# Kernel optimization log

Hardware: AMD Instinct MI355X
Metric: run time of the kernel (lower is better)

## Reference

```python
import jax, jax.numpy as jnp
import numpy as np

D_K = 64
SCALE = 1.0 / (D_K ** 0.5)
NEG = -1.0e9

def setup_inputs() -> dict:
    key = jax.random.key(0)
    kq, kk, kv, km = jax.random.split(key, 4)
    B, H, S, D = 4, 16, 2048, D_K
    query = jax.random.normal(kq, (B, H, S, D), dtype=jnp.float32)
    k_ = jax.random.normal(kk, (B, H, S, D), dtype=jnp.float32)
    v_ = jax.random.normal(kv, (B, H, S, D), dtype=jnp.float32)
    mask = jax.random.randint(km, (B, 1, S, S), 0, 2, dtype=jnp.int32)
    return {"query": query, "key": k_, "value": v_, "mask": mask}

def reference(query, key, value, mask):
    # scores: [B, H, S, S]
    scores = jnp.einsum('bhqd,bhkd->bhqk', query, key) * SCALE
    scores = jnp.where(mask == 0, NEG, scores)
    attn = jax.nn.softmax(scores, axis=-1)
    return jnp.einsum('bhqk,bhkd->bhqd', attn, value)
```

## Files before the change

### kernel.cpp

```cpp
#include <hip/hip_runtime.h>

typedef _Float16 f16x8 __attribute__((ext_vector_type(8)));
typedef _Float16 f16x4 __attribute__((ext_vector_type(4)));
typedef _Float16 f16x2 __attribute__((ext_vector_type(2)));
typedef float    f32x4 __attribute__((ext_vector_type(4)));
typedef unsigned u32x4 __attribute__((ext_vector_type(4)));
typedef unsigned long long u64;

constexpr int Bc = 4, Hc = 16, Sc = 2048, Dc = 64;
constexpr int KVBLK = 64;
constexpr int NKV = Sc / KVBLK;
constexpr int QB  = 256;
constexpr int NQT = Sc / QB;
constexpr int NQ  = 32;

__device__ __forceinline__ float fast_exp2(float x) {
#if __has_builtin(__builtin_amdgcn_exp2f)
  return __builtin_amdgcn_exp2f(x);
#else
  return exp2f(x);
#endif
}

__device__ __forceinline__ void gload16(const void* g, void* l) {
  __builtin_amdgcn_global_load_lds(
      (const __attribute__((address_space(1))) void*)g,
      (__attribute__((address_space(3))) void*)l, 16, 0, 0);
}

__device__ __forceinline__ f32x4 mfma16(f16x8 a, f16x8 b, f32x4 c) {
  return __builtin_amdgcn_mfma_f32_16x16x32_f16(a, b, c, 0, 0, 0);
}

__device__ __forceinline__ unsigned pkrtz(float x, float y) {
  return __builtin_bit_cast(unsigned, __builtin_amdgcn_cvt_pkrtz(x, y));
}

__device__ __forceinline__ float dot2acc(unsigned pk, float acc) {
#if __has_builtin(__builtin_amdgcn_fdot2)
  const f16x2 one2 = {(_Float16)1.f, (_Float16)1.f};
  return __builtin_amdgcn_fdot2(__builtin_bit_cast(f16x2, pk), one2, acc, false);
#else
  const f16x2 v = __builtin_bit_cast(f16x2, pk);
  return acc + (float)v[0] + (float)v[1];
#endif
}

__global__ __launch_bounds__(256)
void cvt_k_sw(const float* __restrict__ K, _Float16* __restrict__ Ko) {
  const int tile = blockIdx.x;
  const int t = threadIdx.x;
  const float* src = K + (size_t)tile * 4096;
  _Float16* dst = Ko + (size_t)tile * 4096;
  #pragma unroll
  for (int cc = 0; cc < 2; ++cc) {
    const int c = t + cc * 256;
    const int r = c >> 3, s = c & 7;
    const int ss = s ^ (r & 7);
    const float* p = src + r * 64 + ss * 8;
    const float4 a = *(const float4*)p;
    const float4 b2 = *(const float4*)(p + 4);
    f16x8 h = {(_Float16)a.x, (_Float16)a.y, (_Float16)a.z, (_Float16)a.w,
               (_Float16)b2.x, (_Float16)b2.y, (_Float16)b2.z, (_Float16)b2.w};
    *(f16x8*)(dst + (size_t)c * 8) = h;
  }
}

__global__ __launch_bounds__(256)
void cvt_v_sw(const float* __restrict__ V, _Float16* __restrict__ Vo) {
  __shared__ float tile[64][65];
  const int tb = blockIdx.x;
  const int t = threadIdx.x;
  const float* src = V + (size_t)tb * 4096;
  {
    const int r = t >> 2, c0 = (t & 3) * 16;
    #pragma unroll
    for (int j = 0; j < 16; j += 4)
      *(float4*)&tile[r][c0 + j] = *(const float4*)(src + r * 64 + c0 + j);
  }
  __syncthreads();
  _Float16* dst = Vo + (size_t)tb * 4096;
  #pragma unroll
  for (int cc = 0; cc < 2; ++cc) {
    const int c = t + cc * 256;
    const int d = c >> 3, ss = c & 7;
    const int m = ss ^ (d & 7);
    const int ks = m >> 2, lg = m & 3;
    f16x8 h;
    #pragma unroll
    for (int e = 0; e < 8; ++e) {
      const int key = 32 * ks + 16 * (e >> 2) + 4 * lg + (e & 3);
      h[e] = (_Float16)tile[key][d];
    }
    *(f16x8*)(dst + (size_t)c * 8) = h;
  }
}

__global__ __launch_bounds__(256)
void pack_mask(const int* __restrict__ M, u64* __restrict__ MB) {
  const int gid  = blockIdx.x * 256 + threadIdx.x;
  const int wv   = gid >> 6, lane = gid & 63;
  const int kv   = wv & (NKV - 1);
  const int row  = (wv >> 5) & (Sc - 1);
  const int b    = wv >> 16;
  const int m    = M[((size_t)b * Sc + row) * Sc + (size_t)kv * 64 + lane];
  const u64 bits = __ballot(m != 0);
  if (lane == 0)
    MB[(((size_t)b * NQ + (row >> 6)) * NKV + kv) * 64 + (row & 63)] = bits;
}

__global__ __launch_bounds__(512, 4)
void attn_fwd11(const float* __restrict__ Q, const _Float16* __restrict__ Ksw,
                const _Float16* __restrict__ Vsw, const u64* __restrict__ MB,
                float* __restrict__ O)
{
  const int bid = (blockIdx.x & 7) * 64 + (blockIdx.x >> 3);
  const int qt  = bid & (NQT - 1);
  const int bh  = bid >> 3;
  const int b   = bh >> 4;
  const int q0  = qt * QB;

  const int tid = threadIdx.x;
  const int w   = tid >> 6;
  const int l   = tid & 63;
  const int lg  = l >> 4;
  const int lc  = l & 15;

  __shared__ _Float16 SB[16384];
  const char* sb = (const char*)SB;

  const int a0 = lc * 128 + (((0 + lg) ^ (lc & 7)) << 4);
  const int a1 = lc * 128 + (((4 + lg) ^ (lc & 7)) << 4);

  f16x8 qf[2][2];
  {
    const float qs = 0.125f * 1.4426950408889634f;
    #pragma unroll
    for (int qa = 0; qa < 2; ++qa) {
      const float* qr = Q + ((size_t)bh * Sc + q0 + w * 32 + qa * 16 + lc) * Dc + 8 * lg;
      #pragma unroll
      for (int ks = 0; ks < 2; ++ks) {
        f16x8 t;
        #pragma unroll
        for (int e = 0; e < 8; ++e) t[e] = (_Float16)(qr[ks * 32 + e] * qs);
        qf[qa][ks] = t;
      }
    }
  }

  f32x4 o_acc[2][4];
  #pragma unroll
  for (int qa = 0; qa < 2; ++qa)
    #pragma unroll
    for (int nt = 0; nt < 4; ++nt) o_acc[qa][nt] = (f32x4){0.f, 0.f, 0.f, 0.f};
  float l_acc0 = 0.f, l_acc1 = 0.f;
  const float NEGL = -1.4426950e9f;

  const char* KswT = (const char*)(Ksw + (size_t)bh * Sc * Dc);
  const char* VswT = (const char*)(Vsw + (size_t)bh * Sc * Dc);
  const int row0 = q0 + w * 32 + lc;
  const int row1 = row0 + 16;
  const u64* Mb0 = MB + ((size_t)(b * NQ + (row0 >> 6)) * NKV) * 64 + (row0 & 63);
  const u64* Mb1 = MB + ((size_t)(b * NQ + (row1 >> 6)) * NKV) * 64 + (row1 & 63);

  auto stage = [&](int kvt, int buf) {
    const char* g = (w < 4) ? KswT + (size_t)kvt * 8192 + w * 2048
                            : VswT + (size_t)kvt * 8192 + (w - 4) * 2048;
    char* lb = (char*)SB + buf * 16384 + ((w < 4) ? w * 2048 : 8192 + (w - 4) * 2048);
    gload16(g + l * 16, lb);
    gload16(g + 1024 + l * 16, lb + 1024);
  };

  auto body = [&](int buf, u64 m0, u64 m1) {
    const int base = buf * 16384;
    f32x4 p[2][4];
    __builtin_amdgcn_s_setprio(1);
    #pragma unroll
    for (int nt = 0; nt < 4; ++nt) {
      const f16x8 k0 = *(const f16x8*)(sb + base + nt * 2048 + a0);
      const f16x8 k1 = *(const f16x8*)(sb + base + nt * 2048 + a1);
      #pragma unroll
      for (int qa = 0; qa < 2; ++qa) {
        f32x4 acc = (f32x4){0.f, 0.f, 0.f, 0.f};
        acc = mfma16(k0, qf[qa][0], acc);
        acc = mfma16(k1, qf[qa][1], acc);
        p[qa][nt] = acc;
      }
    }
    __builtin_amdgcn_s_setprio(0);
    #pragma unroll
    for (int qa = 0; qa < 2; ++qa) {
      const u64 mbits = qa ? m1 : m0;
      #pragma unroll
      for (int nt = 0; nt < 4; ++nt) {
        const unsigned b4 = ((unsigned)(mbits >> (nt * 16 + 4 * lg))) & 0xFu;
        #pragma unroll
        for (int r = 0; r < 4; ++r)
          p[qa][nt][r] = fast_exp2(((b4 >> r) & 1u) ? p[qa][nt][r] : NEGL);
      }
    }
    f16x8 pa0[2], pa1[2];
    #pragma unroll
    for (int qa = 0; qa < 2; ++qa) {
      u32x4 u0, u1;
      #pragma unroll
      for (int i = 0; i < 4; ++i) {
        u0[i] = pkrtz(p[qa][i >> 1][(i & 1) * 2], p[qa][i >> 1][(i & 1) * 2 + 1]);
        u1[i] = pkrtz(p[qa][2 + (i >> 1)][(i & 1) * 2], p[qa][2 + (i >> 1)][(i & 1) * 2 + 1]);
      }
      float la = qa ? l_acc1 : l_acc0;
      #pragma unroll
      for (int i = 0; i < 4; ++i) { la = dot2acc(u0[i], la); la = dot2acc(u1[i], la); }
      if (qa) l_acc1 = la; else l_acc0 = la;
      pa0[qa] = __builtin_bit_cast(f16x8, u0);
      pa1[qa] = __builtin_bit_cast(f16x8, u1);
    }
    __builtin_amdgcn_s_setprio(1);
    #pragma unroll
    for (int nt = 0; nt < 4; ++nt) {
      const f16x8 v0 = *(const f16x8*)(sb + base + 8192 + nt * 2048 + a0);
      const f16x8 v1 = *(const f16x8*)(sb + base + 8192 + nt * 2048 + a1);
      o_acc[0][nt] = mfma16(pa0[0], v0, o_acc[0][nt]);
      o_acc[0][nt] = mfma16(pa1[0], v1, o_acc[0][nt]);
      o_acc[1][nt] = mfma16(pa0[1], v0, o_acc[1][nt]);
      o_acc[1][nt] = mfma16(pa1[1], v1, o_acc[1][nt]);
    }
    __builtin_amdgcn_s_setprio(0);
  };

  u64 mA0 = Mb0[0], mA1 = Mb1[0];
  stage(0, 0);
  asm volatile("s_waitcnt vmcnt(0)" ::: "memory");
  __builtin_amdgcn_sched_barrier(0);
  __builtin_amdgcn_s_barrier();

  u64 mB0, mB1;
  for (int t = 0; t < NKV; t += 2) {
    stage(t + 1, 1);
    mB0 = Mb0[(size_t)(t + 1) * 64];
    mB1 = Mb1[(size_t)(t + 1) * 64];
    asm volatile("s_waitcnt vmcnt(4)" ::: "memory");
    __builtin_amdgcn_sched_barrier(0);
    __builtin_amdgcn_s_barrier();
    body(0, mA0, mA1);
    __builtin_amdgcn_s_barrier();

    if (t + 2 < NKV) {
      stage(t + 2, 0);
      mA0 = Mb0[(size_t)(t + 2) * 64];
      mA1 = Mb1[(size_t)(t + 2) * 64];
      asm volatile("s_waitcnt vmcnt(4)" ::: "memory");
    } else {
      asm volatile("s_waitcnt vmcnt(0)" ::: "memory");
    }
    __builtin_amdgcn_sched_barrier(0);
    __builtin_amdgcn_s_barrier();
    body(1, mB0, mB1);
    __builtin_amdgcn_s_barrier();
  }

  l_acc0 += __shfl_xor(l_acc0, 16, 64);
  l_acc0 += __shfl_xor(l_acc0, 32, 64);
  l_acc1 += __shfl_xor(l_acc1, 16, 64);
  l_acc1 += __shfl_xor(l_acc1, 32, 64);
  #pragma unroll
  for (int qa = 0; qa < 2; ++qa) {
    #pragma unroll
    for (int r = 0; r < 4; ++r) {
      const float li = 1.0f / __shfl(qa ? l_acc1 : l_acc0, 4 * lg + r, 64);
      float* orow = O + ((size_t)bh * Sc + q0 + w * 32 + qa * 16 + 4 * lg + r) * Dc + lc;
      #pragma unroll
      for (int nt = 0; nt < 4; ++nt)
        orow[nt * 16] = o_acc[qa][nt][r] * li;
    }
  }
}

constexpr int LDSW = KVBLK + 8;

__global__ __launch_bounds__(256)
void attn_fwd_v1(const float* __restrict__ Q, const float* __restrict__ K,
                 const float* __restrict__ V, const int* __restrict__ M,
                 float* __restrict__ O)
{
  const int bid   = blockIdx.x;
  const int qtile = bid & 31;
  const int bh    = bid >> 5;
  const int b     = bh >> 4;

  const float* Qp = Q + ((size_t)bh * Sc + (size_t)qtile * 64) * Dc;
  const float* Kp = K + (size_t)bh * Sc * Dc;
  const float* Vp = V + (size_t)bh * Sc * Dc;
  const int*   Mp = M + (size_t)b * Sc * Sc + (size_t)qtile * 64 * Sc;
  float*       Op = O + ((size_t)bh * Sc + (size_t)qtile * 64) * Dc;

  __shared__ _Float16 Klds [KVBLK][LDSW];
  __shared__ _Float16 Vtlds[Dc]   [LDSW];
  __shared__ _Float16 Pl   [64]   [LDSW];

  const int tid = threadIdx.x;
  const int w   = tid >> 6;
  const int l   = tid & 63;
  const int lg  = l >> 4;
  const int lc  = l & 15;

  f16x8 qf[2];
  {
    const float qs = 0.125f * 1.4426950408889634f;
    const float* qrow = Qp + (size_t)(w * 16 + lc) * Dc + 8 * lg;
    #pragma unroll
    for (int ks = 0; ks < 2; ++ks) {
      f16x8 t;
      #pragma unroll
      for (int e = 0; e < 8; ++e) t[e] = (_Float16)(qrow[ks * 32 + e] * qs);
      qf[ks] = t;
    }
  }

  f32x4 o_acc[4];
  #pragma unroll
  for (int nt = 0; nt < 4; ++nt) o_acc[nt] = (f32x4){0.f, 0.f, 0.f, 0.f};
  float m_r[4], l_r[4];
  #pragma unroll
  for (int r = 0; r < 4; ++r) { m_r[r] = -3.0e38f; l_r[r] = 0.f; }
  const float NEGL = -1.4426950e9f;

  for (int kv = 0; kv < NKV; ++kv) {
    const float* Kt = Kp + (size_t)kv * KVBLK * Dc;
    const float* Vt = Vp + (size_t)kv * KVBLK * Dc;
    __syncthreads();
    {
      const int r = tid >> 2, c0 = (tid & 3) * 16;
      const float* src = Kt + (size_t)r * Dc + c0;
      f16x8 h0, h1;
      #pragma unroll
      for (int e = 0; e < 8; ++e) h0[e] = (_Float16)src[e];
      #pragma unroll
      for (int e = 0; e < 8; ++e) h1[e] = (_Float16)src[8 + e];
      *(f16x8*)&Klds[r][c0]     = h0;
      *(f16x8*)&Klds[r][c0 + 8] = h1;
    }
    {
      const int r0 = (tid >> 4) * 4, c0 = (tid & 15) * 4;
      float a_[4][4];
      #pragma unroll
      for (int i = 0; i < 4; ++i) {
        const float4 v4 = *(const float4*)(Vt + (size_t)(r0 + i) * Dc + c0);
        a_[i][0] = v4.x; a_[i][1] = v4.y; a_[i][2] = v4.z; a_[i][3] = v4.w;
      }
      #pragma unroll
      for (int j = 0; j < 4; ++j) {
        f16x4 t = {(_Float16)a_[0][j], (_Float16)a_[1][j],
                   (_Float16)a_[2][j], (_Float16)a_[3][j]};
        *(f16x4*)&Vtlds[c0 + j][r0] = t;
      }
    }
    __syncthreads();

    f32x4 s_acc[4];
    #pragma unroll
    for (int nt = 0; nt < 4; ++nt) {
      f32x4 acc = (f32x4){0.f, 0.f, 0.f, 0.f};
      #pragma unroll
      for (int ks = 0; ks < 2; ++ks) {
        f16x8 kf = *(const f16x8*)&Klds[nt * 16 + lc][ks * 32 + 8 * lg];
        acc = __builtin_amdgcn_mfma_f32_16x16x32_f16(qf[ks], kf, acc, 0, 0, 0);
      }
      s_acc[nt] = acc;
    }

    const int* mbase = Mp + (size_t)kv * KVBLK + lc;
    #pragma unroll
    for (int r = 0; r < 4; ++r) {
      const int qrow = w * 16 + 4 * lg + r;
      const int* mr = mbase + (size_t)qrow * Sc;
      float s0 = (mr[0]  != 0) ? s_acc[0][r] : NEGL;
      float s1 = (mr[16] != 0) ? s_acc[1][r] : NEGL;
      float s2 = (mr[32] != 0) ? s_acc[2][r] : NEGL;
      float s3 = (mr[48] != 0) ? s_acc[3][r] : NEGL;
      float mx = fmaxf(fmaxf(s0, s1), fmaxf(s2, s3));
      #pragma unroll
      for (int off = 1; off < 16; off <<= 1)
        mx = fmaxf(mx, __shfl_xor(mx, off, 64));
      const float mn   = fmaxf(m_r[r], mx);
      const float corr = fast_exp2(m_r[r] - mn);
      m_r[r] = mn;
      float p0 = fast_exp2(s0 - mn);
      float p1 = fast_exp2(s1 - mn);
      float p2 = fast_exp2(s2 - mn);
      float p3 = fast_exp2(s3 - mn);
      float rs = (p0 + p1) + (p2 + p3);
      #pragma unroll
      for (int off = 1; off < 16; off <<= 1)
        rs += __shfl_xor(rs, off, 64);
      l_r[r] = l_r[r] * corr + rs;
      #pragma unroll
      for (int nt = 0; nt < 4; ++nt) o_acc[nt][r] *= corr;
      Pl[qrow][lc]      = (_Float16)p0;
      Pl[qrow][16 + lc] = (_Float16)p1;
      Pl[qrow][32 + lc] = (_Float16)p2;
      Pl[qrow][48 + lc] = (_Float16)p3;
    }

    #pragma unroll
    for (int nt = 0; nt < 4; ++nt) {
      #pragma unroll
      for (int ks = 0; ks < 2; ++ks) {
        f16x8 pf = *(const f16x8*)&Pl[w * 16 + lc][ks * 32 + 8 * lg];
        f16x8 vf = *(const f16x8*)&Vtlds[nt * 16 + lc][ks * 32 + 8 * lg];
        o_acc[nt] = __builtin_amdgcn_mfma_f32_16x16x32_f16(pf, vf, o_acc[nt], 0, 0, 0);
      }
    }
  }

  #pragma unroll
  for (int r = 0; r < 4; ++r) {
    const float inv = 1.0f / l_r[r];
    float* orow = Op + (size_t)(w * 16 + 4 * lg + r) * Dc;
    #pragma unroll
    for (int nt = 0; nt < 4; ++nt)
      orow[nt * 16 + lc] = o_acc[nt][r] * inv;
  }
}

extern "C" void kernel_launch(void* const* d_in, const int* in_sizes, int n_in,
                              void* d_out, int out_size, void* d_ws, size_t ws_size,
                              hipStream_t stream) {
  (void)in_sizes; (void)n_in; (void)out_size;
  const float* Q = (const float*)d_in[0];
  const float* K = (const float*)d_in[1];
  const float* V = (const float*)d_in[2];
  const int*   M = (const int*)d_in[3];
  float*       O = (float*)d_out;

  const size_t nKV      = (size_t)Bc * Hc * Sc * Dc;
  const size_t bytesK16 = nKV * 2;
  const size_t bytesMB  = (size_t)Bc * NQ * NKV * 64 * 8;
  const size_t need     = 2 * bytesK16 + bytesMB;

  if (ws_size >= need) {
    _Float16* K16  = (_Float16*)d_ws;
    _Float16* Vt16 = (_Float16*)((char*)d_ws + bytesK16);
    u64*      MBp  = (u64*)((char*)d_ws + 2 * bytesK16);
    hipLaunchKernelGGL(cvt_k_sw,   dim3(2048),  dim3(256), 0, stream, K, K16);
    hipLaunchKernelGGL(cvt_v_sw,   dim3(2048),  dim3(256), 0, stream, V, Vt16);
    hipLaunchKernelGGL(pack_mask,  dim3(65536), dim3(256), 0, stream, M, MBp);
    hipLaunchKernelGGL(attn_fwd11, dim3(512),   dim3(512), 0, stream, Q, K16, Vt16, MBp, O);
  } else {
    hipLaunchKernelGGL(attn_fwd_v1, dim3(2048), dim3(256), 0, stream, Q, K, V, M, O);
  }
}
```

Baseline: 130.2 us.

## Process 64 query rows per wave with 4-wave blocks to raise K/V reuse

Each block now runs 4 waves instead of 8, and each wave handles 64 query rows (four 16-row groups) instead of 32. Each K/V fragment read from LDS therefore feeds twice as many MFMAs, and every wave stages 4 chunks per tile instead of 2. The aim is to halve LDS read traffic per FLOP and cut barrier and wave overhead. The cost is roughly double the accumulator and score registers per wave and fewer waves to hide latency. The mask loads now use one pointer per wave, covering its 64-row block, instead of one per 16-row group.

```diff
diff --git a/kernel.cpp b/kernel.cpp
--- a/kernel.cpp
+++ b/kernel.cpp
@@ -109,8 +109,8 @@
     MB[(((size_t)b * NQ + (row >> 6)) * NKV + kv) * 64 + (row & 63)] = bits;
 }
 
-__global__ __launch_bounds__(512, 4)
-void attn_fwd11(const float* __restrict__ Q, const _Float16* __restrict__ Ksw,
+__global__ __launch_bounds__(256, 2)
+void attn_fwd13(const float* __restrict__ Q, const _Float16* __restrict__ Ksw,
                 const _Float16* __restrict__ Vsw, const u64* __restrict__ MB,
                 float* __restrict__ O)
 {
@@ -132,12 +132,12 @@
   const int a0 = lc * 128 + (((0 + lg) ^ (lc & 7)) << 4);
   const int a1 = lc * 128 + (((4 + lg) ^ (lc & 7)) << 4);
 
-  f16x8 qf[2][2];
+  f16x8 qf[4][2];
   {
     const float qs = 0.125f * 1.4426950408889634f;
     #pragma unroll
-    for (int qa = 0; qa < 2; ++qa) {
-      const float* qr = Q + ((size_t)bh * Sc + q0 + w * 32 + qa * 16 + lc) * Dc + 8 * lg;
+    for (int qa = 0; qa < 4; ++qa) {
+      const float* qr = Q + ((size_t)bh * Sc + q0 + w * 64 + qa * 16 + lc) * Dc + 8 * lg;
       #pragma unroll
       for (int ks = 0; ks < 2; ++ks) {
         f16x8 t;
@@ -148,39 +148,37 @@
     }
   }
 
-  f32x4 o_acc[2][4];
-  #pragma unroll
-  for (int qa = 0; qa < 2; ++qa)
+  f32x4 o_acc[4][4];
+  #pragma unroll
+  for (int qa = 0; qa < 4; ++qa)
     #pragma unroll
     for (int nt = 0; nt < 4; ++nt) o_acc[qa][nt] = (f32x4){0.f, 0.f, 0.f, 0.f};
-  float l_acc0 = 0.f, l_acc1 = 0.f;
+  float l_acc[4] = {0.f, 0.f, 0.f, 0.f};
   const float NEGL = -1.4426950e9f;
 
   const char* KswT = (const char*)(Ksw + (size_t)bh * Sc * Dc);
   const char* VswT = (const char*)(Vsw + (size_t)bh * Sc * Dc);
-  const int row0 = q0 + w * 32 + lc;
-  const int row1 = row0 + 16;
-  const u64* Mb0 = MB + ((size_t)(b * NQ + (row0 >> 6)) * NKV) * 64 + (row0 & 63);
-  const u64* Mb1 = MB + ((size_t)(b * NQ + (row1 >> 6)) * NKV) * 64 + (row1 & 63);
+  const u64* Mb = MB + ((size_t)(b * NQ + (q0 >> 6) + w) * NKV) * 64 + lc;
 
   auto stage = [&](int kvt, int buf) {
-    const char* g = (w < 4) ? KswT + (size_t)kvt * 8192 + w * 2048
-                            : VswT + (size_t)kvt * 8192 + (w - 4) * 2048;
-    char* lb = (char*)SB + buf * 16384 + ((w < 4) ? w * 2048 : 8192 + (w - 4) * 2048);
-    gload16(g + l * 16, lb);
-    gload16(g + 1024 + l * 16, lb + 1024);
+    const char* g = (w < 2) ? KswT + (size_t)kvt * 8192 + w * 4096
+                            : VswT + (size_t)kvt * 8192 + (w - 2) * 4096;
+    char* lb = (char*)SB + buf * 16384 + ((w < 2) ? w * 4096 : 8192 + (w - 2) * 4096);
+    #pragma unroll
+    for (int j = 0; j < 4; ++j)
+      gload16(g + j * 1024 + l * 16, lb + j * 1024);
   };
 
-  auto body = [&](int buf, u64 m0, u64 m1) {
+  auto body = [&](int buf, u64 m0, u64 m1, u64 m2, u64 m3) {
     const int base = buf * 16384;
-    f32x4 p[2][4];
+    f32x4 p[4][4];
     __builtin_amdgcn_s_setprio(1);
     #pragma unroll
     for (int nt = 0; nt < 4; ++nt) {
       const f16x8 k0 = *(const f16x8*)(sb + base + nt * 2048 + a0);
       const f16x8 k1 = *(const f16x8*)(sb + base + nt * 2048 + a1);
       #pragma unroll
-      for (int qa = 0; qa < 2; ++qa) {
+      for (int qa = 0; qa < 4; ++qa) {
         f32x4 acc = (f32x4){0.f, 0.f, 0.f, 0.f};
         acc = mfma16(k0, qf[qa][0], acc);
         acc = mfma16(k1, qf[qa][1], acc);
@@ -188,9 +186,10 @@
       }
     }
     __builtin_amdgcn_s_setprio(0);
-    #pragma unroll
-    for (int qa = 0; qa < 2; ++qa) {
-      const u64 mbits = qa ? m1 : m0;
+    f16x8 pa0[4], pa1[4];
+    #pragma unroll
+    for (int qa = 0; qa < 4; ++qa) {
+      const u64 mbits = (qa == 0) ? m0 : (qa == 1) ? m1 : (qa == 2) ? m2 : m3;
       #pragma unroll
       for (int nt = 0; nt < 4; ++nt) {
         const unsigned b4 = ((unsigned)(mbits >> (nt * 16 + 4 * lg))) & 0xFu;
@@ -198,20 +197,16 @@
         for (int r = 0; r < 4; ++r)
           p[qa][nt][r] = fast_exp2(((b4 >> r) & 1u) ? p[qa][nt][r] : NEGL);
       }
-    }
-    f16x8 pa0[2], pa1[2];
-    #pragma unroll
-    for (int qa = 0; qa < 2; ++qa) {
       u32x4 u0, u1;
       #pragma unroll
       for (int i = 0; i < 4; ++i) {
         u0[i] = pkrtz(p[qa][i >> 1][(i & 1) * 2], p[qa][i >> 1][(i & 1) * 2 + 1]);
         u1[i] = pkrtz(p[qa][2 + (i >> 1)][(i & 1) * 2], p[qa][2 + (i >> 1)][(i & 1) * 2 + 1]);
       }
-      float la = qa ? l_acc1 : l_acc0;
+      float la = l_acc[qa];
       #pragma unroll
       for (int i = 0; i < 4; ++i) { la = dot2acc(u0[i], la); la = dot2acc(u1[i], la); }
-      if (qa) l_acc1 = la; else l_acc0 = la;
+      l_acc[qa] = la;
       pa0[qa] = __builtin_bit_cast(f16x8, u0);
       pa1[qa] = __builtin_bit_cast(f16x8, u1);
     }
@@ -220,55 +215,57 @@
     for (int nt = 0; nt < 4; ++nt) {
       const f16x8 v0 = *(const f16x8*)(sb + base + 8192 + nt * 2048 + a0);
       const f16x8 v1 = *(const f16x8*)(sb + base + 8192 + nt * 2048 + a1);
-      o_acc[0][nt] = mfma16(pa0[0], v0, o_acc[0][nt]);
-      o_acc[0][nt] = mfma16(pa1[0], v1, o_acc[0][nt]);
-      o_acc[1][nt] = mfma16(pa0[1], v0, o_acc[1][nt]);
-      o_acc[1][nt] = mfma16(pa1[1], v1, o_acc[1][nt]);
+      #pragma unroll
+      for (int qa = 0; qa < 4; ++qa) {
+        o_acc[qa][nt] = mfma16(pa0[qa], v0, o_acc[qa][nt]);
+        o_acc[qa][nt] = mfma16(pa1[qa], v1, o_acc[qa][nt]);
+      }
     }
     __builtin_amdgcn_s_setprio(0);
   };
 
-  u64 mA0 = Mb0[0], mA1 = Mb1[0];
+  u64 mA0 = Mb[0], mA1 = Mb[16], mA2 = Mb[32], mA3 = Mb[48];
   stage(0, 0);
   asm volatile("s_waitcnt vmcnt(0)" ::: "memory");
   __builtin_amdgcn_sched_barrier(0);
   __builtin_amdgcn_s_barrier();
 
-  u64 mB0, mB1;
+  u64 mB0, mB1, mB2, mB3;
   for (int t = 0; t < NKV; t += 2) {
     stage(t + 1, 1);
-    mB0 = Mb0[(size_t)(t + 1) * 64];
-    mB1 = Mb1[(size_t)(t + 1) * 64];
-    asm volatile("s_waitcnt vmcnt(4)" ::: "memory");
+    {
+      const size_t mo = (size_t)(t + 1) * 64;
+      mB0 = Mb[mo]; mB1 = Mb[mo + 16]; mB2 = Mb[mo + 32]; mB3 = Mb[mo + 48];
+    }
+    asm volatile("s_waitcnt vmcnt(8)" ::: "memory");
     __builtin_amdgcn_sched_barrier(0);
     __builtin_amdgcn_s_barrier();
-    body(0, mA0, mA1);
+    body(0, mA0, mA1, mA2, mA3);
     __builtin_amdgcn_s_barrier();
 
     if (t + 2 < NKV) {
       stage(t + 2, 0);
-      mA0 = Mb0[(size_t)(t + 2) * 64];
-      mA1 = Mb1[(size_t)(t + 2) * 64];
-      asm volatile("s_waitcnt vmcnt(4)" ::: "memory");
+      const size_t mo = (size_t)(t + 2) * 64;
+      mA0 = Mb[mo]; mA1 = Mb[mo + 16]; mA2 = Mb[mo + 32]; mA3 = Mb[mo + 48];
+      asm volatile("s_waitcnt vmcnt(8)" ::: "memory");
     } else {
       asm volatile("s_waitcnt vmcnt(0)" ::: "memory");
     }
     __builtin_amdgcn_sched_barrier(0);
     __builtin_amdgcn_s_barrier();
-    body(1, mB0, mB1);
+    body(1, mB0, mB1, mB2, mB3);
     __builtin_amdgcn_s_barrier();
   }
 
-  l_acc0 += __shfl_xor(l_acc0, 16, 64);
-  l_acc0 += __shfl_xor(l_acc0, 32, 64);
-  l_acc1 += __shfl_xor(l_acc1, 16, 64);
-  l_acc1 += __shfl_xor(l_acc1, 32, 64);
-  #pragma unroll
-  for (int qa = 0; qa < 2; ++qa) {
+  #pragma unroll
+  for (int qa = 0; qa < 4; ++qa) {
+    float la = l_acc[qa];
+    la += __shfl_xor(la, 16, 64);
+    la += __shfl_xor(la, 32, 64);
     #pragma unroll
     for (int r = 0; r < 4; ++r) {
-      const float li = 1.0f / __shfl(qa ? l_acc1 : l_acc0, 4 * lg + r, 64);
-      float* orow = O + ((size_t)bh * Sc + q0 + w * 32 + qa * 16 + 4 * lg + r) * Dc + lc;
+      const float li = 1.0f / __shfl(la, 4 * lg + r, 64);
+      float* orow = O + ((size_t)bh * Sc + q0 + w * 64 + qa * 16 + 4 * lg + r) * Dc + lc;
       #pragma unroll
       for (int nt = 0; nt < 4; ++nt)
         orow[nt * 16] = o_acc[qa][nt][r] * li;
@@ -445,7 +442,7 @@
     hipLaunchKernelGGL(cvt_k_sw,   dim3(2048),  dim3(256), 0, stream, K, K16);
     hipLaunchKernelGGL(cvt_v_sw,   dim3(2048),  dim3(256), 0, stream, V, Vt16);
     hipLaunchKernelGGL(pack_mask,  dim3(65536), dim3(256), 0, stream, M, MBp);
-    hipLaunchKernelGGL(attn_fwd11, dim3(512),   dim3(512), 0, stream, Q, K16, Vt16, MBp, O);
+    hipLaunchKernelGGL(attn_fwd13, dim3(512),   dim3(256), 0, stream, Q, K16, Vt16, MBp, O);
   } else {
     hipLaunchKernelGGL(attn_fwd_v1, dim3(2048), dim3(256), 0, stream, Q, K, V, M, O);
   }
```

After: 137.7 us. +5.8%, slower.
